# Kernel optimization log

Measured on AMD Instinct MI355X. Metric: run time of the kernel, lower is better.

## Reference

```python
import jax, jax.numpy as jnp
import numpy as np

N, E, F, H, OUT, PROP_STEPS, NUM_LAYERS = 50000, 800000, 64, 128, 32, 3, 2


def setup_inputs() -> dict:
    key = jax.random.key(0)
    ks = jax.random.split(key, 24)
    def lin(kw, kb, out_d, in_d):
        s = 1.0 / np.sqrt(in_d)
        w = jax.random.uniform(kw, (out_d, in_d), jnp.float32, -s, s)
        b = jax.random.uniform(kb, (out_d,), jnp.float32, -s, s)
        return w, b
    enc_w, enc_b = lin(ks[0], ks[1], 1, 2)
    ratt_w, ratt_b = lin(ks[2], ks[3], 1, F)
    iatt_w, iatt_b = lin(ks[4], ks[5], 1, F)
    rlin0_w, rlin0_b = lin(ks[6], ks[7], H, F)
    rlin1_w, rlin1_b = lin(ks[8], ks[9], H, H)
    ilin0_w, ilin0_b = lin(ks[10], ks[11], H, F)
    ilin1_w, ilin1_b = lin(ks[12], ks[13], H, H)
    out_w, out_b = lin(ks[14], ks[15], OUT, 2 * H)
    return {
        'real_feature': jax.random.normal(ks[16], (N, F), jnp.float32),
        'imag_feature': jax.random.normal(ks[17], (N, F), jnp.float32),
        'edge_entropy': jax.random.uniform(ks[18], (E,), jnp.float32),
        'edge_cluster_coefficient': jax.random.uniform(ks[19], (E,), jnp.float32),
        'edge_weight_sym': jax.random.uniform(ks[20], (E,), jnp.float32),
        'exp_weight_q': jnp.asarray(0.5, jnp.float32),
        'enc_w': enc_w, 'enc_b': enc_b,
        'ratt_w': ratt_w, 'ratt_b': ratt_b,
        'iatt_w': iatt_w, 'iatt_b': iatt_b,
        'rlin0_w': rlin0_w, 'rlin0_b': rlin0_b,
        'rlin1_w': rlin1_w, 'rlin1_b': rlin1_b,
        'ilin0_w': ilin0_w, 'ilin0_b': ilin0_b,
        'ilin1_w': ilin1_w, 'ilin1_b': ilin1_b,
        'out_w': out_w, 'out_b': out_b,
        'row': jax.random.randint(ks[21], (E,), 0, N, jnp.int32),
        'col': jax.random.randint(ks[22], (E,), 0, N, jnp.int32),
    }


def reference(real_feature, imag_feature, edge_entropy, edge_cluster_coefficient,
              edge_weight_sym, exp_weight_q, enc_w, enc_b, ratt_w, ratt_b,
              iatt_w, iatt_b, rlin0_w, rlin0_b, rlin1_w, rlin1_b,
              ilin0_w, ilin0_b, ilin1_w, ilin1_b, out_w, out_b, row, col):
    n = real_feature.shape[0]
    # structural encoding -> complex phase per edge (soft_label is None branch)
    structure_info = jnp.stack((edge_entropy, edge_cluster_coefficient), axis=1)  # [E,2]
    se = (structure_info @ enc_w.T + enc_b).reshape(-1)                            # [E]
    phase = exp_weight_q * se
    wr = edge_weight_sym * jnp.cos(phase)  # real adj values
    wi = edge_weight_sym * jnp.sin(phase)  # imag adj values

    reals, imags = [real_feature], [imag_feature]
    for _ in range(PROP_STEPS):
        xr = reals[-1][col]  # [E,F] gather once, shared by both SpMMs
        xi = imags[-1][col]
        # complex SpMM: (wr + i*wi) * (xr + i*xi)
        msg_r = wr[:, None] * xr - wi[:, None] * xi
        msg_i = wi[:, None] * xr + wr[:, None] * xi
        reals.append(jax.ops.segment_sum(msg_r, row, num_segments=n))
        imags.append(jax.ops.segment_sum(msg_i, row, num_segments=n))

    R = jnp.stack(reals)  # [S+1, N, F]
    I = jnp.stack(imags)

    # attention pooling over prop steps (softmax over step axis, per node)
    ra = R @ ratt_w.T + ratt_b  # [S+1, N, 1]
    ia = I @ iatt_w.T + iatt_b
    rw = jax.nn.softmax(jax.nn.sigmoid(ra[..., 0]), axis=0)  # [S+1, N]
    iw = jax.nn.softmax(jax.nn.sigmoid(ia[..., 0]), axis=0)
    real_x = jnp.einsum('snf,sn->nf', R, rw)
    imag_x = jnp.einsum('snf,sn->nf', I, iw)

    # complex MLP with ComReLU (mask both parts by sign of real part); dropout=0 -> identity
    for (rw_, rb_, iw_, ib_) in ((rlin0_w, rlin0_b, ilin0_w, ilin0_b),
                                 (rlin1_w, rlin1_b, ilin1_w, ilin1_b)):
        zr = real_x @ rw_.T + rb_
        zi = imag_x @ iw_.T + ib_
        mask = (zr >= 0).astype(zr.dtype)
        real_x, imag_x = zr * mask, zi * mask

    x = jnp.concatenate((real_x, imag_x), axis=-1)
    return x @ out_w.T + out_b
```

## Files before the change

### kernel.cpp

```cpp
#include <hip/hip_runtime.h>

#define N_NODES 50000
#define N_EDGES 800000
#define FDIM 64
#define NST 50000
#define SA_BLOCKS ((N_NODES + 1023) / 1024)


__global__ __launch_bounds__(256) void hist_kernel(const int* __restrict__ row,
                                                   int* __restrict__ cnt, int E) {
  int e = blockIdx.x * 256 + threadIdx.x;
  if (e < E) atomicAdd(&cnt[row[e]], 1);
}

__global__ __launch_bounds__(1024) void scanA_kernel(const int* __restrict__ cnt,
                                                     int* __restrict__ offs,
                                                     int* __restrict__ bsum,
                                                     int n) {
  __shared__ int s[1024];
  int t = threadIdx.x;
  int i = blockIdx.x * 1024 + t;
  int v = (i < n) ? cnt[i] : 0;
  s[t] = v;
  __syncthreads();
  for (int d = 1; d < 1024; d <<= 1) {
    int add = (t >= d) ? s[t - d] : 0;
    __syncthreads();
    s[t] += add;
    __syncthreads();
  }
  if (i < n) offs[i] = s[t] - v;
  if (t == 1023) bsum[blockIdx.x] = s[1023];
}

__global__ __launch_bounds__(64) void scanB_kernel(int* __restrict__ bsum,
                                                   int* __restrict__ boff,
                                                   int nb) {
  __shared__ int s[64];
  int t = threadIdx.x;
  int v = (t < nb) ? bsum[t] : 0;
  s[t] = v;
  __syncthreads();
  for (int d = 1; d < 64; d <<= 1) {
    int add = (t >= d) ? s[t - d] : 0;
    __syncthreads();
    s[t] += add;
    __syncthreads();
  }
  if (t < nb) boff[t] = s[t] - v;
}

__global__ __launch_bounds__(1024) void scanC_kernel(int* __restrict__ offs,
                                                     int* __restrict__ cursor,
                                                     const int* __restrict__ boff,
                                                     int n, int E) {
  int t = threadIdx.x;
  int i = blockIdx.x * 1024 + t;
  int bo = boff[blockIdx.x];
  if (i < n) {
    int o = offs[i] + bo;
    offs[i] = o;
    cursor[i] = o;
  }
  if (i == 0) offs[n] = E;
}

__global__ __launch_bounds__(256) void scatter_kernel(
    const int* __restrict__ row, const int* __restrict__ col,
    const float* __restrict__ ent, const float* __restrict__ ccf,
    const float* __restrict__ wsym, const float* __restrict__ encw,
    const float* __restrict__ encb, const float* __restrict__ q,
    int* __restrict__ cursor, int* __restrict__ col_s,
    float2* __restrict__ ws, int E) {
  int e = blockIdx.x * 256 + threadIdx.x;
  if (e >= E) return;
  float se = encw[0] * ent[e] + encw[1] * ccf[e] + encb[0];
  float ph = q[0] * se;
  float sw, cw;
  sincosf(ph, &sw, &cw);
  float w = wsym[e];
  int pos = atomicAdd(&cursor[row[e]], 1);
  col_s[pos] = col[e];
  ws[pos] = make_float2(w * cw, w * sw);
}


__global__ __launch_bounds__(256) void prep_weights(
    const float* __restrict__ r0, const float* __restrict__ i0,
    const float* __restrict__ r1, const float* __restrict__ i1,
    float* __restrict__ r0T, float* __restrict__ i0T, float* __restrict__ r1T,
    float* __restrict__ i1T) {
  int t = blockIdx.x * 256 + threadIdx.x;
  if (t < 128 * 64) {
    int h = t / 64, f = t % 64;
    r0T[f * 128 + h] = r0[t];
    i0T[f * 128 + h] = i0[t];
  }
  if (t < 128 * 128) {
    int h = t / 128, f = t % 128;
    r1T[f * 128 + h] = r1[t];
    i1T[f * 128 + h] = i1[t];
  }
}


__global__ __launch_bounds__(256) void pack_kernel(const float* __restrict__ re,
                                                   const float* __restrict__ im,
                                                   float2* __restrict__ X,
                                                   int total) {
  int i = blockIdx.x * 256 + threadIdx.x;
  if (i < total) X[i] = make_float2(re[i], im[i]);
}


__global__ __launch_bounds__(256) void prop_kernel(
    const float* __restrict__ X, float* __restrict__ Y,
    const int* __restrict__ offs, const int* __restrict__ col_s,
    const float2* __restrict__ ws, int n) {
  int wave = (int)((blockIdx.x * (size_t)blockDim.x + threadIdx.x) >> 6);
  int lane = threadIdx.x & 63;
  if (wave >= n) return;
  int beg = __builtin_amdgcn_readfirstlane(offs[wave]);
  int end = __builtin_amdgcn_readfirstlane(offs[wave + 1]);
  const float2* Xl = (const float2*)X + lane;
  float2 acc = make_float2(0.f, 0.f);
  int j = beg;
  for (; j + 8 <= end; j += 8) {
    int c[8];
#pragma unroll
    for (int k = 0; k < 8; ++k) c[k] = col_s[j + k];
    float2 x[8];
#pragma unroll
    for (int k = 0; k < 8; ++k) x[k] = Xl[(size_t)c[k] * 64];
#pragma unroll
    for (int k = 0; k < 8; ++k) {
      float2 w = ws[j + k];
      acc.x += w.x * x[k].x - w.y * x[k].y;
      acc.y += w.y * x[k].x + w.x * x[k].y;
    }
  }
  int rem = end - j;
  if (rem > 0) {
    int c[8];
#pragma unroll
    for (int k = 0; k < 8; ++k)
      if (k < rem) c[k] = col_s[j + k];
    float2 x[8];
#pragma unroll
    for (int k = 0; k < 8; ++k)
      if (k < rem) x[k] = Xl[(size_t)c[k] * 64];
#pragma unroll
    for (int k = 0; k < 8; ++k)
      if (k < rem) {
        float2 w = ws[j + k];
        acc.x += w.x * x[k].x - w.y * x[k].y;
        acc.y += w.y * x[k].x + w.x * x[k].y;
      }
  }
  ((float2*)Y)[(size_t)wave * 64 + lane] = acc;
}


__device__ __forceinline__ float wave_sum(float v) {
#pragma unroll
  for (int d = 32; d > 0; d >>= 1) v += __shfl_xor(v, d, 64);
  return v;
}

__global__ __launch_bounds__(256) void pool_kernel(
    const float* __restrict__ R0f, const float* __restrict__ I0f,
    const float* __restrict__ X1, const float* __restrict__ X2,
    const float* __restrict__ X3, const float* __restrict__ rattw,
    const float* __restrict__ rattb, const float* __restrict__ iattw,
    const float* __restrict__ iattb, float* __restrict__ PT, int n) {
  __shared__ float pt[128 * 65];
  int wid = threadIdx.x >> 6, lane = threadIdx.x & 63;
  int nb = blockIdx.x * 64;
  float aw = rattw[lane], bw = iattw[lane];
  float rb0 = rattb[0], ib0 = iattb[0];
  for (int k = 0; k < 16; ++k) {
    int ln = wid * 16 + k;
    int nc = min(nb + ln, n - 1);
    float r0 = R0f[(size_t)nc * 64 + lane];
    float q0 = I0f[(size_t)nc * 64 + lane];
    size_t base = (size_t)nc * 128 + 2 * lane;
    float2 v1 = *(const float2*)&X1[base];
    float2 v2 = *(const float2*)&X2[base];
    float2 v3 = *(const float2*)&X3[base];
    float ra0 = wave_sum(r0 * aw) + rb0;
    float ra1 = wave_sum(v1.x * aw) + rb0;
    float ra2 = wave_sum(v2.x * aw) + rb0;
    float ra3 = wave_sum(v3.x * aw) + rb0;
    float ia0 = wave_sum(q0 * bw) + ib0;
    float ia1 = wave_sum(v1.y * bw) + ib0;
    float ia2 = wave_sum(v2.y * bw) + ib0;
    float ia3 = wave_sum(v3.y * bw) + ib0;
    float s0 = 1.f / (1.f + __expf(-ra0));
    float s1 = 1.f / (1.f + __expf(-ra1));
    float s2 = 1.f / (1.f + __expf(-ra2));
    float s3 = 1.f / (1.f + __expf(-ra3));
    float t0 = 1.f / (1.f + __expf(-ia0));
    float t1 = 1.f / (1.f + __expf(-ia1));
    float t2 = 1.f / (1.f + __expf(-ia2));
    float t3 = 1.f / (1.f + __expf(-ia3));
    float mR = fmaxf(fmaxf(s0, s1), fmaxf(s2, s3));
    float e0 = __expf(s0 - mR), e1 = __expf(s1 - mR), e2 = __expf(s2 - mR),
          e3 = __expf(s3 - mR);
    float invR = 1.f / (e0 + e1 + e2 + e3);
    float mI = fmaxf(fmaxf(t0, t1), fmaxf(t2, t3));
    float g0 = __expf(t0 - mI), g1 = __expf(t1 - mI), g2 = __expf(t2 - mI),
          g3 = __expf(t3 - mI);
    float invI = 1.f / (g0 + g1 + g2 + g3);
    float pr = (r0 * e0 + v1.x * e1 + v2.x * e2 + v3.x * e3) * invR;
    float pi = (q0 * g0 + v1.y * g1 + v2.y * g2 + v3.y * g3) * invI;
    pt[lane * 65 + ln] = pr;
    pt[(64 + lane) * 65 + ln] = pi;
  }
  __syncthreads();
  int c = threadIdx.x & 63, fr = threadIdx.x >> 6;
  for (int r = 0; r < 32; ++r) {
    int f = fr * 32 + r;
    int nd = nb + c;
    if (nd < n) PT[(size_t)f * NST + nd] = pt[f * 65 + c];
  }
}


__global__ __launch_bounds__(512, 8) void mlp_kernel(
    const float* __restrict__ PT, const float* __restrict__ r0T,
    const float* __restrict__ r0b, const float* __restrict__ i0T,
    const float* __restrict__ i0b, const float* __restrict__ r1T,
    const float* __restrict__ r1b, const float* __restrict__ i1T,
    const float* __restrict__ i1b, const float* __restrict__ ow,
    const float* __restrict__ ob, float* __restrict__ out, int n) {
  __shared__ float zt[64 * 132];
  int lane = threadIdx.x & 63;
  int wid = threadIdx.x >> 6;
  int h0 = __builtin_amdgcn_readfirstlane(wid * 16);
  int nb = blockIdx.x * 64;
  int node = min(nb + lane, n - 1);
  float* zrow = &zt[lane * 132];

  float zr[16], zi[16];
#pragma unroll
  for (int j = 0; j < 16; ++j) {
    zr[j] = r0b[h0 + j];
    zi[j] = i0b[h0 + j];
  }
#pragma unroll 2
  for (int f = 0; f < 64; ++f) {
    float ar = PT[(size_t)f * NST + node];
    float ai = PT[(size_t)(64 + f) * NST + node];
    const float* wr = &r0T[f * 128 + h0];
    const float* wi = &i0T[f * 128 + h0];
#pragma unroll
    for (int j = 0; j < 16; ++j) {
      zr[j] += ar * wr[j];
      zi[j] += ai * wi[j];
    }
  }
#pragma unroll
  for (int j = 0; j < 16; ++j) {
    float m = (zr[j] >= 0.f) ? 1.f : 0.f;
    zr[j] *= m;
    zi[j] *= m;
  }

#pragma unroll
  for (int j4 = 0; j4 < 4; ++j4)
    *(float4*)&zrow[h0 + 4 * j4] = make_float4(zr[4 * j4], zr[4 * j4 + 1],
                                               zr[4 * j4 + 2], zr[4 * j4 + 3]);
  __syncthreads();
  float yr[16];
#pragma unroll
  for (int j = 0; j < 16; ++j) yr[j] = r1b[h0 + j];
#pragma unroll 2
  for (int f4 = 0; f4 < 32; ++f4) {
    float4 a4 = *(const float4*)&zrow[4 * f4];
    const float* w0 = &r1T[(4 * f4) * 128 + h0];
    const float* w1 = &r1T[(4 * f4 + 1) * 128 + h0];
    const float* w2 = &r1T[(4 * f4 + 2) * 128 + h0];
    const float* w3 = &r1T[(4 * f4 + 3) * 128 + h0];
#pragma unroll
    for (int j = 0; j < 16; ++j)
      yr[j] += a4.x * w0[j] + a4.y * w1[j] + a4.z * w2[j] + a4.w * w3[j];
  }
  __syncthreads();

#pragma unroll
  for (int j4 = 0; j4 < 4; ++j4)
    *(float4*)&zrow[h0 + 4 * j4] = make_float4(zi[4 * j4], zi[4 * j4 + 1],
                                               zi[4 * j4 + 2], zi[4 * j4 + 3]);
  __syncthreads();
  float yi[16];
#pragma unroll
  for (int j = 0; j < 16; ++j) yi[j] = i1b[h0 + j];
#pragma unroll 2
  for (int f4 = 0; f4 < 32; ++f4) {
    float4 a4 = *(const float4*)&zrow[4 * f4];
    const float* w0 = &i1T[(4 * f4) * 128 + h0];
    const float* w1 = &i1T[(4 * f4 + 1) * 128 + h0];
    const float* w2 = &i1T[(4 * f4 + 2) * 128 + h0];
    const float* w3 = &i1T[(4 * f4 + 3) * 128 + h0];
#pragma unroll
    for (int j = 0; j < 16; ++j)
      yi[j] += a4.x * w0[j] + a4.y * w1[j] + a4.z * w2[j] + a4.w * w3[j];
  }
#pragma unroll
  for (int j = 0; j < 16; ++j) {
    float m = (yr[j] >= 0.f) ? 1.f : 0.f;
    yr[j] *= m;
    yi[j] *= m;
  }
  __syncthreads();

  int o0 = __builtin_amdgcn_readfirstlane(wid * 4);
  float os[4] = {0.f, 0.f, 0.f, 0.f};
#pragma unroll
  for (int j4 = 0; j4 < 4; ++j4)
    *(float4*)&zrow[h0 + 4 * j4] = make_float4(yr[4 * j4], yr[4 * j4 + 1],
                                               yr[4 * j4 + 2], yr[4 * j4 + 3]);
  __syncthreads();
#pragma unroll 2
  for (int f4 = 0; f4 < 32; ++f4) {
    float4 v = *(const float4*)&zrow[4 * f4];
#pragma unroll
    for (int oo = 0; oo < 4; ++oo) {
      const float* w = &ow[(o0 + oo) * 256 + 4 * f4];
      os[oo] += v.x * w[0] + v.y * w[1] + v.z * w[2] + v.w * w[3];
    }
  }
  __syncthreads();
#pragma unroll
  for (int j4 = 0; j4 < 4; ++j4)
    *(float4*)&zrow[h0 + 4 * j4] = make_float4(yi[4 * j4], yi[4 * j4 + 1],
                                               yi[4 * j4 + 2], yi[4 * j4 + 3]);
  __syncthreads();
#pragma unroll 2
  for (int f4 = 0; f4 < 32; ++f4) {
    float4 v = *(const float4*)&zrow[4 * f4];
#pragma unroll
    for (int oo = 0; oo < 4; ++oo) {
      const float* w = &ow[(o0 + oo) * 256 + 128 + 4 * f4];
      os[oo] += v.x * w[0] + v.y * w[1] + v.z * w[2] + v.w * w[3];
    }
  }
#pragma unroll
  for (int oo = 0; oo < 4; ++oo)
    out[(size_t)node * 32 + o0 + oo] = os[oo] + ob[o0 + oo];
}


extern "C" void kernel_launch(void* const* d_in, const int* in_sizes, int n_in,
                              void* d_out, int out_size, void* d_ws,
                              size_t ws_size, hipStream_t stream) {
  const float* realf = (const float*)d_in[0];
  const float* imagf = (const float*)d_in[1];
  const float* ent = (const float*)d_in[2];
  const float* ccf = (const float*)d_in[3];
  const float* wsym = (const float*)d_in[4];
  const float* q = (const float*)d_in[5];
  const float* encw = (const float*)d_in[6];
  const float* encb = (const float*)d_in[7];
  const float* rattw = (const float*)d_in[8];
  const float* rattb = (const float*)d_in[9];
  const float* iattw = (const float*)d_in[10];
  const float* iattb = (const float*)d_in[11];
  const float* r0w = (const float*)d_in[12];
  const float* r0b = (const float*)d_in[13];
  const float* r1w = (const float*)d_in[14];
  const float* r1b = (const float*)d_in[15];
  const float* i0w = (const float*)d_in[16];
  const float* i0b = (const float*)d_in[17];
  const float* i1w = (const float*)d_in[18];
  const float* i1b = (const float*)d_in[19];
  const float* ow = (const float*)d_in[20];
  const float* ob = (const float*)d_in[21];
  const int* row = (const int*)d_in[22];
  const int* col = (const int*)d_in[23];
  float* out = (float*)d_out;

  char* p = (char*)d_ws;
  auto alloc = [&](size_t bytes) -> void* {
    void* r = (void*)p;
    p += (bytes + 255) & ~(size_t)255;
    return r;
  };
  int* cnt = (int*)alloc(N_NODES * sizeof(int));
  int* offs = (int*)alloc((N_NODES + 1) * sizeof(int));
  int* bsum = (int*)alloc(SA_BLOCKS * sizeof(int));
  int* boff = (int*)alloc(SA_BLOCKS * sizeof(int));
  int* col_s = (int*)alloc(N_EDGES * sizeof(int));
  float2* ws2 = (float2*)alloc(N_EDGES * sizeof(float2));
  size_t NX = (size_t)N_NODES * 128 * sizeof(float);
  float* X0 = (float*)alloc(NX);
  float* X1 = (float*)alloc(NX);
  float* X2 = (float*)alloc(NX);
  float* X3 = (float*)alloc(NX);
  float* PT = (float*)alloc((size_t)128 * NST * sizeof(float));
  float* r0T = (float*)alloc(64 * 128 * 4);
  float* i0T = (float*)alloc(64 * 128 * 4);
  float* r1T = (float*)alloc(128 * 128 * 4);
  float* i1T = (float*)alloc(128 * 128 * 4);

  hipMemsetAsync(cnt, 0, N_NODES * sizeof(int), stream);
  prep_weights<<<64, 256, 0, stream>>>(r0w, i0w, r1w, i1w, r0T, i0T, r1T, i1T);
  hist_kernel<<<(N_EDGES + 255) / 256, 256, 0, stream>>>(row, cnt, N_EDGES);
  scanA_kernel<<<SA_BLOCKS, 1024, 0, stream>>>(cnt, offs, bsum, N_NODES);
  scanB_kernel<<<1, 64, 0, stream>>>(bsum, boff, SA_BLOCKS);
  scanC_kernel<<<SA_BLOCKS, 1024, 0, stream>>>(offs, cnt, boff, N_NODES,
                                               N_EDGES);
  scatter_kernel<<<(N_EDGES + 255) / 256, 256, 0, stream>>>(
      row, col, ent, ccf, wsym, encw, encb, q, cnt, col_s, ws2, N_EDGES);
  pack_kernel<<<(N_NODES * 64 + 255) / 256, 256, 0, stream>>>(
      realf, imagf, (float2*)X0, N_NODES * 64);

  const int pgrid = (N_NODES + 3) / 4;
  prop_kernel<<<pgrid, 256, 0, stream>>>(X0, X1, offs, col_s, ws2, N_NODES);
  prop_kernel<<<pgrid, 256, 0, stream>>>(X1, X2, offs, col_s, ws2, N_NODES);
  prop_kernel<<<pgrid, 256, 0, stream>>>(X2, X3, offs, col_s, ws2, N_NODES);

  const int hgrid = (N_NODES + 63) / 64;
  pool_kernel<<<hgrid, 256, 0, stream>>>(realf, imagf, X1, X2, X3, rattw,
                                         rattb, iattw, iattb, PT, N_NODES);
  mlp_kernel<<<hgrid, 512, 0, stream>>>(PT, r0T, r0b, i0T, i0b, r1T, r1b, i1T,
                                        i1b, ow, ob, out, N_NODES);
}
```

Measured before the change: 425.3 us.

## Fuse attention pooling into MLP head kernel via shared memory

Merges the pooling kernel and the MLP kernel into one launch. Pooled features stay in shared memory instead of going through a transposed global PT buffer, which removes that buffer's write and read round trip and one launch. The 512-thread block now does 8 nodes per wave in the pooling phase and reuses one shared buffer for both phases, which needs an extra barrier.

Measured after the change: 404.8 us. 4.8% less time.

```diff
diff --git a/kernel.cpp b/kernel.cpp
--- a/kernel.cpp
+++ b/kernel.cpp
@@ -3,7 +3,6 @@
 #define N_NODES 50000
 #define N_EDGES 800000
 #define FDIM 64
-#define NST 50000
 #define SA_BLOCKS ((N_NODES + 1023) / 1024)
 
 
@@ -167,80 +166,67 @@
   return v;
 }
 
-__global__ __launch_bounds__(256) void pool_kernel(
+__global__ __launch_bounds__(512, 8) void fused_head(
     const float* __restrict__ R0f, const float* __restrict__ I0f,
     const float* __restrict__ X1, const float* __restrict__ X2,
     const float* __restrict__ X3, const float* __restrict__ rattw,
     const float* __restrict__ rattb, const float* __restrict__ iattw,
-    const float* __restrict__ iattb, float* __restrict__ PT, int n) {
-  __shared__ float pt[128 * 65];
-  int wid = threadIdx.x >> 6, lane = threadIdx.x & 63;
-  int nb = blockIdx.x * 64;
-  float aw = rattw[lane], bw = iattw[lane];
-  float rb0 = rattb[0], ib0 = iattb[0];
-  for (int k = 0; k < 16; ++k) {
-    int ln = wid * 16 + k;
-    int nc = min(nb + ln, n - 1);
-    float r0 = R0f[(size_t)nc * 64 + lane];
-    float q0 = I0f[(size_t)nc * 64 + lane];
-    size_t base = (size_t)nc * 128 + 2 * lane;
-    float2 v1 = *(const float2*)&X1[base];
-    float2 v2 = *(const float2*)&X2[base];
-    float2 v3 = *(const float2*)&X3[base];
-    float ra0 = wave_sum(r0 * aw) + rb0;
-    float ra1 = wave_sum(v1.x * aw) + rb0;
-    float ra2 = wave_sum(v2.x * aw) + rb0;
-    float ra3 = wave_sum(v3.x * aw) + rb0;
-    float ia0 = wave_sum(q0 * bw) + ib0;
-    float ia1 = wave_sum(v1.y * bw) + ib0;
-    float ia2 = wave_sum(v2.y * bw) + ib0;
-    float ia3 = wave_sum(v3.y * bw) + ib0;
-    float s0 = 1.f / (1.f + __expf(-ra0));
-    float s1 = 1.f / (1.f + __expf(-ra1));
-    float s2 = 1.f / (1.f + __expf(-ra2));
-    float s3 = 1.f / (1.f + __expf(-ra3));
-    float t0 = 1.f / (1.f + __expf(-ia0));
-    float t1 = 1.f / (1.f + __expf(-ia1));
-    float t2 = 1.f / (1.f + __expf(-ia2));
-    float t3 = 1.f / (1.f + __expf(-ia3));
-    float mR = fmaxf(fmaxf(s0, s1), fmaxf(s2, s3));
-    float e0 = __expf(s0 - mR), e1 = __expf(s1 - mR), e2 = __expf(s2 - mR),
-          e3 = __expf(s3 - mR);
-    float invR = 1.f / (e0 + e1 + e2 + e3);
-    float mI = fmaxf(fmaxf(t0, t1), fmaxf(t2, t3));
-    float g0 = __expf(t0 - mI), g1 = __expf(t1 - mI), g2 = __expf(t2 - mI),
-          g3 = __expf(t3 - mI);
-    float invI = 1.f / (g0 + g1 + g2 + g3);
-    float pr = (r0 * e0 + v1.x * e1 + v2.x * e2 + v3.x * e3) * invR;
-    float pi = (q0 * g0 + v1.y * g1 + v2.y * g2 + v3.y * g3) * invI;
-    pt[lane * 65 + ln] = pr;
-    pt[(64 + lane) * 65 + ln] = pi;
-  }
-  __syncthreads();
-  int c = threadIdx.x & 63, fr = threadIdx.x >> 6;
-  for (int r = 0; r < 32; ++r) {
-    int f = fr * 32 + r;
-    int nd = nb + c;
-    if (nd < n) PT[(size_t)f * NST + nd] = pt[f * 65 + c];
-  }
-}
-
-
-__global__ __launch_bounds__(512, 8) void mlp_kernel(
-    const float* __restrict__ PT, const float* __restrict__ r0T,
+    const float* __restrict__ iattb, const float* __restrict__ r0T,
     const float* __restrict__ r0b, const float* __restrict__ i0T,
     const float* __restrict__ i0b, const float* __restrict__ r1T,
     const float* __restrict__ r1b, const float* __restrict__ i1T,
     const float* __restrict__ i1b, const float* __restrict__ ow,
     const float* __restrict__ ob, float* __restrict__ out, int n) {
-  __shared__ float zt[64 * 132];
+  __shared__ float buf[8448];
   int lane = threadIdx.x & 63;
   int wid = threadIdx.x >> 6;
+  int nb = blockIdx.x * 64;
+
+  {
+    float aw = rattw[lane], bw = iattw[lane];
+    float rb0 = rattb[0], ib0 = iattb[0];
+    for (int k = 0; k < 8; ++k) {
+      int ln = wid * 8 + k;
+      int nc = min(nb + ln, n - 1);
+      float r0 = R0f[(size_t)nc * 64 + lane];
+      float q0 = I0f[(size_t)nc * 64 + lane];
+      size_t base = (size_t)nc * 128 + 2 * lane;
+      float2 v1 = *(const float2*)&X1[base];
+      float2 v2 = *(const float2*)&X2[base];
+      float2 v3 = *(const float2*)&X3[base];
+      float ra0 = wave_sum(r0 * aw) + rb0;
+      float ra1 = wave_sum(v1.x * aw) + rb0;
+      float ra2 = wave_sum(v2.x * aw) + rb0;
+      float ra3 = wave_sum(v3.x * aw) + rb0;
+      float ia0 = wave_sum(q0 * bw) + ib0;
+      float ia1 = wave_sum(v1.y * bw) + ib0;
+      float ia2 = wave_sum(v2.y * bw) + ib0;
+      float ia3 = wave_sum(v3.y * bw) + ib0;
+      float s0 = 1.f / (1.f + __expf(-ra0));
+      float s1 = 1.f / (1.f + __expf(-ra1));
+      float s2 = 1.f / (1.f + __expf(-ra2));
+      float s3 = 1.f / (1.f + __expf(-ra3));
+      float t0 = 1.f / (1.f + __expf(-ia0));
+      float t1 = 1.f / (1.f + __expf(-ia1));
+      float t2 = 1.f / (1.f + __expf(-ia2));
+      float t3 = 1.f / (1.f + __expf(-ia3));
+      float mR = fmaxf(fmaxf(s0, s1), fmaxf(s2, s3));
+      float e0 = __expf(s0 - mR), e1 = __expf(s1 - mR), e2 = __expf(s2 - mR),
+            e3 = __expf(s3 - mR);
+      float invR = 1.f / (e0 + e1 + e2 + e3);
+      float mI = fmaxf(fmaxf(t0, t1), fmaxf(t2, t3));
+      float g0 = __expf(t0 - mI), g1 = __expf(t1 - mI), g2 = __expf(t2 - mI),
+            g3 = __expf(t3 - mI);
+      float invI = 1.f / (g0 + g1 + g2 + g3);
+      float pr = (r0 * e0 + v1.x * e1 + v2.x * e2 + v3.x * e3) * invR;
+      float pi = (q0 * g0 + v1.y * g1 + v2.y * g2 + v3.y * g3) * invI;
+      buf[lane * 65 + ln] = pr;
+      buf[(64 + lane) * 65 + ln] = pi;
+    }
+  }
+  __syncthreads();
+
   int h0 = __builtin_amdgcn_readfirstlane(wid * 16);
-  int nb = blockIdx.x * 64;
-  int node = min(nb + lane, n - 1);
-  float* zrow = &zt[lane * 132];
-
   float zr[16], zi[16];
 #pragma unroll
   for (int j = 0; j < 16; ++j) {
@@ -249,8 +235,8 @@
   }
 #pragma unroll 2
   for (int f = 0; f < 64; ++f) {
-    float ar = PT[(size_t)f * NST + node];
-    float ai = PT[(size_t)(64 + f) * NST + node];
+    float ar = buf[f * 65 + lane];
+    float ai = buf[(64 + f) * 65 + lane];
     const float* wr = &r0T[f * 128 + h0];
     const float* wi = &i0T[f * 128 + h0];
 #pragma unroll
@@ -265,6 +251,9 @@
     zr[j] *= m;
     zi[j] *= m;
   }
+  __syncthreads();
+
+  float* zrow = &buf[lane * 132];
 
 #pragma unroll
   for (int j4 = 0; j4 < 4; ++j4)
@@ -314,6 +303,7 @@
   }
   __syncthreads();
 
+  int node = min(nb + lane, n - 1);
   int o0 = __builtin_amdgcn_readfirstlane(wid * 4);
   float os[4] = {0.f, 0.f, 0.f, 0.f};
 #pragma unroll
@@ -397,7 +387,6 @@
   float* X1 = (float*)alloc(NX);
   float* X2 = (float*)alloc(NX);
   float* X3 = (float*)alloc(NX);
-  float* PT = (float*)alloc((size_t)128 * NST * sizeof(float));
   float* r0T = (float*)alloc(64 * 128 * 4);
   float* i0T = (float*)alloc(64 * 128 * 4);
   float* r1T = (float*)alloc(128 * 128 * 4);
@@ -421,8 +410,7 @@
   prop_kernel<<<pgrid, 256, 0, stream>>>(X2, X3, offs, col_s, ws2, N_NODES);
 
   const int hgrid = (N_NODES + 63) / 64;
-  pool_kernel<<<hgrid, 256, 0, stream>>>(realf, imagf, X1, X2, X3, rattw,
-                                         rattb, iattw, iattb, PT, N_NODES);
-  mlp_kernel<<<hgrid, 512, 0, stream>>>(PT, r0T, r0b, i0T, i0b, r1T, r1b, i1T,
-                                        i1b, ow, ob, out, N_NODES);
-}
+  fused_head<<<hgrid, 512, 0, stream>>>(realf, imagf, X1, X2, X3, rattw, rattb,
+                                        iattw, iattb, r0T, r0b, i0T, i0b, r1T,
+                                        r1b, i1T, i1b, ow, ob, out, N_NODES);
+}
```
